# Kernel tuning notes

Measured on AMD Instinct MI355X. Metric: run time of the kernel, lower is better.

Reference implementation:

```python
import jax, jax.numpy as jnp
import numpy as np

B, S, D, H = 1, 2048, 1024, 16
DH = D // H  # 64
ROPE_THETA = 10000.0


def _rope_tables(seq_len, half_dim, theta):
    inv = 1.0 / (theta ** (np.arange(0, half_dim, dtype=np.float32) / half_dim))
    ang = np.arange(seq_len, dtype=np.float32)[:, None] * inv[None, :]
    return jnp.asarray(np.cos(ang)), jnp.asarray(np.sin(ang))


def setup_inputs() -> dict:
    key = jax.random.key(0)
    ks = jax.random.split(key, 6)
    x = jax.random.normal(ks[0], (B, S, D), dtype=jnp.float32)
    # block-diagonal mask over ~4 packed images -> sorted segment ids
    seg_ids = jnp.sort(jax.random.randint(ks[1], (S,), 0, 4, dtype=jnp.int32))
    freqs_cos, freqs_sin = _rope_tables(S, DH // 2, ROPE_THETA)
    scale = 1.0 / np.sqrt(D)
    wq = jax.random.normal(ks[2], (D, D), dtype=jnp.float32) * scale
    wk = jax.random.normal(ks[3], (D, D), dtype=jnp.float32) * scale
    wv = jax.random.normal(ks[4], (D, D), dtype=jnp.float32) * scale
    wo = jax.random.normal(ks[5], (D, D), dtype=jnp.float32) * scale
    return {"x": x, "seg_ids": seg_ids, "freqs_cos": freqs_cos,
            "freqs_sin": freqs_sin, "wq": wq, "wk": wk, "wv": wv, "wo": wo}


def _apply_rope(t, cos, sin):
    # t: [B,S,H,DH]; interpret last dim as DH//2 complex pairs (real, imag)
    tr = t.reshape(B, S, H, DH // 2, 2)
    a, b = tr[..., 0], tr[..., 1]
    c = cos[None, :, None, :]  # [1,S,1,DH/2]
    s = sin[None, :, None, :]
    out = jnp.stack([a * c - b * s, a * s + b * c], axis=-1)
    return out.reshape(B, S, H, DH)


def reference(x, seg_ids, freqs_cos, freqs_sin, wq, wk, wv, wo):
    q = (x @ wq.T).reshape(B, S, H, DH)
    k = (x @ wk.T).reshape(B, S, H, DH)
    v = (x @ wv.T).reshape(B, S, H, DH)
    q = _apply_rope(q, freqs_cos, freqs_sin)
    k = _apply_rope(k, freqs_cos, freqs_sin)
    scores = jnp.einsum('bqhd,bkhd->bhqk', q, k) / np.float32(np.sqrt(DH))
    block_mask = (seg_ids[:, None] == seg_ids[None, :])  # [S,S] block-diagonal
    scores = jnp.where(block_mask[None, None], scores, jnp.float32(-1e9))
    attn = jax.nn.softmax(scores, axis=-1)
    out = jnp.einsum('bhqk,bkhd->bqhd', attn, v).reshape(B, S, D)
    return out @ wo.T
```

## Files before the change

kernel.cpp:

```cpp
#include <hip/hip_runtime.h>

typedef __bf16 bf16;
typedef __bf16 bf16x4 __attribute__((ext_vector_type(4)));
typedef __bf16 bf16x8 __attribute__((ext_vector_type(8)));
typedef float  f32x4  __attribute__((ext_vector_type(4)));

#define S_LEN 2048
#define D_DIM 1024
#define NHEAD 16
#define DHEAD 64

__device__ __forceinline__ void async_cp16(const bf16* g, bf16* l) {
  __builtin_amdgcn_global_load_lds(
      (__attribute__((address_space(1))) void*)(void*)g,
      (__attribute__((address_space(3))) void*)l,
      16, 0, 0);
}

__global__ __launch_bounds__(256) void cvt_k(
    const float* __restrict__ x,  const float* __restrict__ w0,
    const float* __restrict__ w1, const float* __restrict__ w2,
    const float* __restrict__ w3, bf16* __restrict__ dst)
{
  int i = blockIdx.x * 256 + threadIdx.x;
  const float* src;
  int off;
  if (i < (1 << 18)) {
    src = x; off = i;
  } else {
    int j = i - (1 << 18);
    int s = j >> 17;
    off = j & ((1 << 17) - 1);
    src = (s == 0) ? w0 : (s == 1) ? w1 : (s == 2) ? w2 : w3;
  }
  f32x4 a = *(const f32x4*)(src + (size_t)off * 8);
  f32x4 b = *(const f32x4*)(src + (size_t)off * 8 + 4);
  bf16x8 o;
  o[0] = (bf16)a[0]; o[1] = (bf16)a[1]; o[2] = (bf16)a[2]; o[3] = (bf16)a[3];
  o[4] = (bf16)b[0]; o[5] = (bf16)b[1]; o[6] = (bf16)b[2]; o[7] = (bf16)b[3];
  *((bf16x8*)dst + i) = o;
}

template <typename OutT>
__global__ __launch_bounds__(256) void gemm_bt(
    const bf16* __restrict__ A,
    const bf16* __restrict__ B0, const bf16* __restrict__ B1,
    const bf16* __restrict__ B2,
    OutT* __restrict__ Cbase)
{
  constexpr int K = 1024, N = 1024;
  const int z = blockIdx.z;
  const bf16* W = (z == 0) ? B0 : (z == 1) ? B1 : B2;
  OutT* C = Cbase + (size_t)z * 2048 * 1024;

  __shared__ bf16 As[128 * 32] __attribute__((aligned(16)));
  __shared__ bf16 Bs[64 * 32] __attribute__((aligned(16)));

  const int t = threadIdx.x;
  const int lane = t & 63;
  const int w = t >> 6;
  const int lm = lane & 15, lq = lane >> 4;
  const int wr = w >> 1, wc = w & 1;
  const int bm = blockIdx.y, bn = blockIdx.x;

  const bf16* Abase = A + (size_t)bm * 128 * K;
  const bf16* Wbase = W + (size_t)bn * 64 * K;

  f32x4 acc[4][2] = {};

  for (int kk = 0; kk < K; kk += 32) {
#pragma unroll
    for (int i = 0; i < 2; ++i) {
      int c = w * 128 + i * 64 + lane;
      int row = c >> 2, kc = (c & 3) * 8;
      async_cp16(Abase + (size_t)row * K + kk + kc, As + (w * 2 + i) * 512);
    }
    {
      int c = w * 64 + lane;
      int row = c >> 2, kc = (c & 3) * 8;
      async_cp16(Wbase + (size_t)row * K + kk + kc, Bs + w * 512);
    }
    __syncthreads();

    bf16x8 af[4], bfr[2];
#pragma unroll
    for (int mi = 0; mi < 4; ++mi)
      af[mi] = *(const bf16x8*)&As[(wr * 64 + mi * 16 + lm) * 32 + lq * 8];
#pragma unroll
    for (int ni = 0; ni < 2; ++ni)
      bfr[ni] = *(const bf16x8*)&Bs[(wc * 32 + ni * 16 + lm) * 32 + lq * 8];
#pragma unroll
    for (int mi = 0; mi < 4; ++mi)
#pragma unroll
      for (int ni = 0; ni < 2; ++ni)
        acc[mi][ni] = __builtin_amdgcn_mfma_f32_16x16x32_bf16(
            af[mi], bfr[ni], acc[mi][ni], 0, 0, 0);
    __syncthreads();
  }

#pragma unroll
  for (int mi = 0; mi < 4; ++mi)
#pragma unroll
    for (int ni = 0; ni < 2; ++ni) {
      int col = bn * 64 + wc * 32 + ni * 16 + lm;
#pragma unroll
      for (int r = 0; r < 4; ++r) {
        int row = bm * 128 + wr * 64 + mi * 16 + lq * 4 + r;
        C[(size_t)row * N + col] = (OutT)acc[mi][ni][r];
      }
    }
}

__global__ __launch_bounds__(256) void prep_k(
    bf16* __restrict__ q, bf16* __restrict__ k,
    const bf16* __restrict__ v, bf16* __restrict__ vt,
    const float* __restrict__ cosT, const float* __restrict__ sinT,
    const int* __restrict__ seg, int* __restrict__ kbr)
{
  __shared__ bf16 tile[64 * 65];
  __shared__ int firstv[4];
  const int b = blockIdx.x;
  const int t = threadIdx.x;

  if (b < 1024) {
    bf16* ptr = (b < 512) ? q : k;
    float scale = (b < 512) ? 0.125f : 1.0f;
    int tid = (b & 511) * 256 + t;
    int s = tid >> 6;
    int u = tid & 63;
    int h = u >> 2, qq = u & 3;
    bf16* base = ptr + (size_t)s * D_DIM + h * DHEAD + qq * 16;
    bf16x8 lo = *(const bf16x8*)base;
    bf16x8 hi = *(const bf16x8*)(base + 8);
    f32x4 c0 = *(const f32x4*)(cosT + s * 32 + qq * 8);
    f32x4 c1 = *(const f32x4*)(cosT + s * 32 + qq * 8 + 4);
    f32x4 s0 = *(const f32x4*)(sinT + s * 32 + qq * 8);
    f32x4 s1 = *(const f32x4*)(sinT + s * 32 + qq * 8 + 4);
    bf16x8 olo, ohi;
#pragma unroll
    for (int j = 0; j < 4; ++j) {
      float a = (float)lo[2 * j], bb = (float)lo[2 * j + 1];
      olo[2 * j]     = (bf16)((a * c0[j] - bb * s0[j]) * scale);
      olo[2 * j + 1] = (bf16)((a * s0[j] + bb * c0[j]) * scale);
      float a2 = (float)hi[2 * j], b2 = (float)hi[2 * j + 1];
      ohi[2 * j]     = (bf16)((a2 * c1[j] - b2 * s1[j]) * scale);
      ohi[2 * j + 1] = (bf16)((a2 * s1[j] + b2 * c1[j]) * scale);
    }
    *(bf16x8*)base = olo;
    *(bf16x8*)(base + 8) = ohi;
  } else if (b < 1536) {
    int b2 = b - 1024;
    const int s0t = (b2 & 31) * 64;
    const int d0t = (b2 >> 5) * 64;
    const int c = t & 63, r0 = t >> 6;
#pragma unroll
    for (int r = r0; r < 64; r += 4)
      tile[r * 65 + c] = v[(size_t)(s0t + r) * D_DIM + d0t + c];
    __syncthreads();
#pragma unroll
    for (int r = r0; r < 64; r += 4)
      vt[(size_t)(d0t + r) * S_LEN + s0t + c] = tile[c * 65 + r];
  } else {
    if (t < 4) firstv[t] = S_LEN;
    __syncthreads();
    for (int i = t; i < S_LEN; i += 256) {
      int s = seg[i];
      if (i == 0 || seg[i - 1] != s) atomicMin(&firstv[s], i);
    }
    __syncthreads();
    if (t < 32) {
      int smin = seg[t * 64], smax = seg[t * 64 + 63];
      int lb = S_LEN, ub = S_LEN;
      for (int vv = smin; vv < 4; ++vv) lb = min(lb, firstv[vv]);
      for (int vv = smax + 1; vv < 4; ++vv) ub = min(ub, firstv[vv]);
      kbr[t * 2] = lb >> 6;
      kbr[t * 2 + 1] = (ub - 1) >> 6;
    }
  }
}

__global__ __launch_bounds__(256) void attn_k(
    const bf16* __restrict__ Q, const bf16* __restrict__ Kmat,
    const bf16* __restrict__ Vt, const int* __restrict__ seg,
    const int* __restrict__ kbr,
    float* __restrict__ Opar, float* __restrict__ Lpar)
{
  __shared__ bf16 Ks[64 * 72] __attribute__((aligned(16)));
  __shared__ bf16 Vs[64 * 72] __attribute__((aligned(16)));
  __shared__ bf16 Ps[4][16 * 72] __attribute__((aligned(16)));
  __shared__ int segk[64];

  const int h = blockIdx.y;
  const int qt = blockIdx.x & 31, par = blockIdx.x >> 5;
  const int q0 = qt * 64;
  const int t = threadIdx.x, lane = t & 63, w = t >> 6;
  const int lm = lane & 15, lq = lane >> 4;
  const int qrow = q0 + w * 16;

  const int kb0f = kbr[qt * 2], kb1f = kbr[qt * 2 + 1];

  bf16x8 qf[2];
#pragma unroll
  for (int ks = 0; ks < 2; ++ks)
    qf[ks] = *(const bf16x8*)(Q + (size_t)(qrow + lm) * D_DIM + h * DHEAD +
                              ks * 32 + lq * 8);

  int sq[4];
  float l_i[4];
#pragma unroll
  for (int r = 0; r < 4; ++r) {
    sq[r] = seg[qrow + lq * 4 + r];
    l_i[r] = 0.0f;
  }
  f32x4 o[4] = {};

  const int srow0 = t >> 3, sch = (t & 7) * 8;
  const int srow1 = (256 + t) >> 3;

  const int kbS = kb0f + par;
  f32x4 pk0, pk1, pv0, pv1;
  int psg;
  if (kbS <= kb1f) {
    const int k0 = kbS * 64;
    pk0 = *(const f32x4*)(Kmat + (size_t)(k0 + srow0) * D_DIM + h * DHEAD + sch);
    pk1 = *(const f32x4*)(Kmat + (size_t)(k0 + srow1) * D_DIM + h * DHEAD + sch);
    pv0 = *(const f32x4*)(Vt + (size_t)(h * DHEAD + srow0) * S_LEN + k0 + sch);
    pv1 = *(const f32x4*)(Vt + (size_t)(h * DHEAD + srow1) * S_LEN + k0 + sch);
    if (t < 64) psg = seg[k0 + t];
  }

  for (int kb = kbS; kb <= kb1f; kb += 2) {
    __syncthreads();
    *(f32x4*)&Ks[srow0 * 72 + sch] = pk0;
    *(f32x4*)&Ks[srow1 * 72 + sch] = pk1;
    *(f32x4*)&Vs[srow0 * 72 + sch] = pv0;
    *(f32x4*)&Vs[srow1 * 72 + sch] = pv1;
    if (t < 64) segk[t] = psg;
    __syncthreads();

    if (kb + 2 <= kb1f) {
      const int k0 = (kb + 2) * 64;
      pk0 = *(const f32x4*)(Kmat + (size_t)(k0 + srow0) * D_DIM + h * DHEAD + sch);
      pk1 = *(const f32x4*)(Kmat + (size_t)(k0 + srow1) * D_DIM + h * DHEAD + sch);
      pv0 = *(const f32x4*)(Vt + (size_t)(h * DHEAD + srow0) * S_LEN + k0 + sch);
      pv1 = *(const f32x4*)(Vt + (size_t)(h * DHEAD + srow1) * S_LEN + k0 + sch);
      if (t < 64) psg = seg[k0 + t];
    }

    f32x4 sa[4] = {};
#pragma unroll
    for (int ks = 0; ks < 2; ++ks) {
      bf16x8 kf[4];
#pragma unroll
      for (int ni = 0; ni < 4; ++ni)
        kf[ni] = *(const bf16x8*)&Ks[(ni * 16 + lm) * 72 + ks * 32 + lq * 8];
#pragma unroll
      for (int ni = 0; ni < 4; ++ni)
        sa[ni] = __builtin_amdgcn_mfma_f32_16x16x32_bf16(qf[ks], kf[ni],
                                                         sa[ni], 0, 0, 0);
    }

    int sk[4];
#pragma unroll
    for (int ni = 0; ni < 4; ++ni) sk[ni] = segk[ni * 16 + lm];

#pragma unroll
    for (int r = 0; r < 4; ++r)
#pragma unroll
      for (int ni = 0; ni < 4; ++ni) {
        float p = (sq[r] == sk[ni]) ? __expf(sa[ni][r]) : 0.0f;
        l_i[r] += p;
        Ps[w][(lq * 4 + r) * 72 + ni * 16 + lm] = (bf16)p;
      }

#pragma unroll
    for (int ks = 0; ks < 2; ++ks) {
      bf16x8 pf = *(const bf16x8*)&Ps[w][lm * 72 + ks * 32 + lq * 8];
      bf16x8 vf[4];
#pragma unroll
      for (int ni = 0; ni < 4; ++ni)
        vf[ni] = *(const bf16x8*)&Vs[(ni * 16 + lm) * 72 + ks * 32 + lq * 8];
#pragma unroll
      for (int ni = 0; ni < 4; ++ni)
        o[ni] = __builtin_amdgcn_mfma_f32_16x16x32_bf16(pf, vf[ni], o[ni],
                                                        0, 0, 0);
    }
  }

  float* Ob = Opar + ((size_t)(par * NHEAD + h) * S_LEN) * DHEAD;
  float* Lb = Lpar + (size_t)(par * NHEAD + h) * S_LEN;
#pragma unroll
  for (int r = 0; r < 4; ++r) {
    float l = l_i[r];
    l += __shfl_xor(l, 1);
    l += __shfl_xor(l, 2);
    l += __shfl_xor(l, 4);
    l += __shfl_xor(l, 8);
    int row = qrow + lq * 4 + r;
    if (lm == 0) Lb[row] = l;
#pragma unroll
    for (int ni = 0; ni < 4; ++ni)
      Ob[(size_t)row * DHEAD + ni * 16 + lm] = o[ni][r];
  }
}

__global__ __launch_bounds__(256) void combine_k(
    const float* __restrict__ Opar, const float* __restrict__ Lpar,
    bf16* __restrict__ AO)
{
  int idx = blockIdx.x * 256 + threadIdx.x;
  int c4 = idx & 15;
  int rh = idx >> 4;
  int row = rh & 2047;
  int h = rh >> 11;
  const size_t PO = (size_t)NHEAD * S_LEN * DHEAD;
  const float* o0 = Opar + ((size_t)h * S_LEN + row) * DHEAD + c4 * 4;
  f32x4 a = *(const f32x4*)o0;
  f32x4 b = *(const f32x4*)(o0 + PO);
  float l = Lpar[(size_t)h * S_LEN + row] +
            Lpar[(size_t)NHEAD * S_LEN + (size_t)h * S_LEN + row];
  float inv = 1.0f / l;
  bf16x4 ov;
#pragma unroll
  for (int j = 0; j < 4; ++j) ov[j] = (bf16)((a[j] + b[j]) * inv);
  *(bf16x4*)(AO + (size_t)row * D_DIM + h * DHEAD + c4 * 4) = ov;
}

extern "C" void kernel_launch(void* const* d_in, const int* in_sizes, int n_in,
                              void* d_out, int out_size, void* d_ws,
                              size_t ws_size, hipStream_t stream)
{
  const float* x  = (const float*)d_in[0];
  const int*   sg = (const int*)d_in[1];
  const float* fc = (const float*)d_in[2];
  const float* fs = (const float*)d_in[3];
  const float* wq = (const float*)d_in[4];
  const float* wk = (const float*)d_in[5];
  const float* wv = (const float*)d_in[6];
  const float* wo = (const float*)d_in[7];
  float* out = (float*)d_out;

  const size_t MAT = (size_t)S_LEN * D_DIM;
  const size_t WSZ = (size_t)D_DIM * D_DIM;
  bf16* xb  = (bf16*)d_ws;
  bf16* wqb = xb + MAT;
  bf16* wkb = wqb + WSZ;
  bf16* wvb = wkb + WSZ;
  bf16* wob = wvb + WSZ;
  bf16* q0  = wob + WSZ;
  bf16* k0  = q0 + MAT;
  bf16* v0  = k0 + MAT;
  bf16* vt  = v0 + MAT;
  bf16* ao  = vt + MAT;
  float* opar = (float*)(ao + MAT);
  float* lpar = opar + 2 * MAT;
  int*   kbr  = (int*)(lpar + 2 * NHEAD * S_LEN);

  dim3 blk(256);
  cvt_k<<<dim3(3072), blk, 0, stream>>>(x, wq, wk, wv, wo, xb);
  gemm_bt<bf16><<<dim3(16, 16, 3), blk, 0, stream>>>(xb, wqb, wkb, wvb, q0);
  prep_k<<<dim3(1537), blk, 0, stream>>>(q0, k0, v0, vt, fc, fs, sg, kbr);
  attn_k<<<dim3(64, 16), blk, 0, stream>>>(q0, k0, vt, sg, kbr, opar, lpar);
  combine_k<<<dim3(2048), blk, 0, stream>>>(opar, lpar, ao);
  gemm_bt<float><<<dim3(16, 16, 1), blk, 0, stream>>>(ao, wob, wob, wob, out);
}
```

Before: 158.5 us.

## Fuse RoPE into QKV GEMM epilogue, widen K-step, split-K output projection

RoPE rotation and the Q scale move into the QKV GEMM epilogue, using a lane shuffle to fetch the paired column, so the separate read-modify-write pass over Q and K is gone. Both GEMMs now stage 64-wide K chunks in two LDS buffers per barrier, which halves the number of sync points. The output projection is split-K over two z-slices and accumulates with fp32 atomics into a zeroed output, doubling its grid to fill more CUs. The cost is an extra memset plus atomic traffic and a nondeterministic summation order.

```diff
diff --git a/kernel.cpp b/kernel.cpp
--- a/kernel.cpp
+++ b/kernel.cpp
@@ -41,20 +41,22 @@
   *((bf16x8*)dst + i) = o;
 }
 
-template <typename OutT>
-__global__ __launch_bounds__(256) void gemm_bt(
+__global__ __launch_bounds__(256) void gemm_qkv(
     const bf16* __restrict__ A,
     const bf16* __restrict__ B0, const bf16* __restrict__ B1,
     const bf16* __restrict__ B2,
-    OutT* __restrict__ Cbase)
+    const float* __restrict__ cosT, const float* __restrict__ sinT,
+    bf16* __restrict__ Cbase)
 {
   constexpr int K = 1024, N = 1024;
   const int z = blockIdx.z;
   const bf16* W = (z == 0) ? B0 : (z == 1) ? B1 : B2;
-  OutT* C = Cbase + (size_t)z * 2048 * 1024;
-
-  __shared__ bf16 As[128 * 32] __attribute__((aligned(16)));
-  __shared__ bf16 Bs[64 * 32] __attribute__((aligned(16)));
+  bf16* C = Cbase + (size_t)z * 2048 * 1024;
+
+  __shared__ bf16 As0[128 * 32] __attribute__((aligned(16)));
+  __shared__ bf16 As1[128 * 32] __attribute__((aligned(16)));
+  __shared__ bf16 Bs0[64 * 32] __attribute__((aligned(16)));
+  __shared__ bf16 Bs1[64 * 32] __attribute__((aligned(16)));
 
   const int t = threadIdx.x;
   const int lane = t & 63;
@@ -68,33 +70,140 @@
 
   f32x4 acc[4][2] = {};
 
-  for (int kk = 0; kk < K; kk += 32) {
-#pragma unroll
-    for (int i = 0; i < 2; ++i) {
-      int c = w * 128 + i * 64 + lane;
-      int row = c >> 2, kc = (c & 3) * 8;
-      async_cp16(Abase + (size_t)row * K + kk + kc, As + (w * 2 + i) * 512);
+  for (int kk = 0; kk < K; kk += 64) {
+#pragma unroll
+    for (int g = 0; g < 2; ++g) {
+      int c = (w * 2 + g) * 64 + lane;
+      int row = c >> 2, k8 = c & 3;
+      const bf16* ga = Abase + (size_t)row * K + kk + k8 * 8;
+      async_cp16(ga, As0 + (w * 2 + g) * 512);
+      async_cp16(ga + 32, As1 + (w * 2 + g) * 512);
     }
     {
       int c = w * 64 + lane;
-      int row = c >> 2, kc = (c & 3) * 8;
-      async_cp16(Wbase + (size_t)row * K + kk + kc, Bs + w * 512);
-    }
-    __syncthreads();
-
-    bf16x8 af[4], bfr[2];
+      int row = c >> 2, k8 = c & 3;
+      const bf16* gb = Wbase + (size_t)row * K + kk + k8 * 8;
+      async_cp16(gb, Bs0 + w * 512);
+      async_cp16(gb + 32, Bs1 + w * 512);
+    }
+    __syncthreads();
+
+#pragma unroll
+    for (int ks = 0; ks < 2; ++ks) {
+      const bf16* As = ks ? As1 : As0;
+      const bf16* Bs = ks ? Bs1 : Bs0;
+      bf16x8 af[4], bfr[2];
+#pragma unroll
+      for (int mi = 0; mi < 4; ++mi)
+        af[mi] = *(const bf16x8*)&As[(wr * 64 + mi * 16 + lm) * 32 + lq * 8];
+#pragma unroll
+      for (int ni = 0; ni < 2; ++ni)
+        bfr[ni] = *(const bf16x8*)&Bs[(wc * 32 + ni * 16 + lm) * 32 + lq * 8];
+#pragma unroll
+      for (int mi = 0; mi < 4; ++mi)
+#pragma unroll
+        for (int ni = 0; ni < 2; ++ni)
+          acc[mi][ni] = __builtin_amdgcn_mfma_f32_16x16x32_bf16(
+              af[mi], bfr[ni], acc[mi][ni], 0, 0, 0);
+    }
+    __syncthreads();
+  }
+
+  if (z < 2) {
+    const float scale = (z == 0) ? 0.125f : 1.0f;
 #pragma unroll
     for (int mi = 0; mi < 4; ++mi)
-      af[mi] = *(const bf16x8*)&As[(wr * 64 + mi * 16 + lm) * 32 + lq * 8];
-#pragma unroll
-    for (int ni = 0; ni < 2; ++ni)
-      bfr[ni] = *(const bf16x8*)&Bs[(wc * 32 + ni * 16 + lm) * 32 + lq * 8];
+#pragma unroll
+      for (int ni = 0; ni < 2; ++ni) {
+        int gcol = bn * 64 + wc * 32 + ni * 16 + lm;
+        int p = (gcol & 63) >> 1;
+        bool even = (gcol & 1) == 0;
+#pragma unroll
+        for (int r = 0; r < 4; ++r) {
+          int row = bm * 128 + wr * 64 + mi * 16 + lq * 4 + r;
+          float v = acc[mi][ni][r];
+          float mate = __shfl_xor(v, 1);
+          float cv = cosT[row * 32 + p];
+          float sv = sinT[row * 32 + p];
+          float res = even ? (v * cv - mate * sv) : (mate * sv + v * cv);
+          C[(size_t)row * N + gcol] = (bf16)(res * scale);
+        }
+      }
+  } else {
 #pragma unroll
     for (int mi = 0; mi < 4; ++mi)
 #pragma unroll
+      for (int ni = 0; ni < 2; ++ni) {
+        int gcol = bn * 64 + wc * 32 + ni * 16 + lm;
+#pragma unroll
+        for (int r = 0; r < 4; ++r) {
+          int row = bm * 128 + wr * 64 + mi * 16 + lq * 4 + r;
+          C[(size_t)row * N + gcol] = (bf16)acc[mi][ni][r];
+        }
+      }
+  }
+}
+
+__global__ __launch_bounds__(256) void gemm_wo(
+    const bf16* __restrict__ A, const bf16* __restrict__ W,
+    float* __restrict__ C)
+{
+  constexpr int K = 1024, N = 1024;
+  const int z = blockIdx.z;
+
+  __shared__ bf16 As0[128 * 32] __attribute__((aligned(16)));
+  __shared__ bf16 As1[128 * 32] __attribute__((aligned(16)));
+  __shared__ bf16 Bs0[64 * 32] __attribute__((aligned(16)));
+  __shared__ bf16 Bs1[64 * 32] __attribute__((aligned(16)));
+
+  const int t = threadIdx.x;
+  const int lane = t & 63;
+  const int w = t >> 6;
+  const int lm = lane & 15, lq = lane >> 4;
+  const int wr = w >> 1, wc = w & 1;
+  const int bm = blockIdx.y, bn = blockIdx.x;
+
+  const bf16* Abase = A + (size_t)bm * 128 * K;
+  const bf16* Wbase = W + (size_t)bn * 64 * K;
+
+  f32x4 acc[4][2] = {};
+
+  for (int kk = z * 512; kk < z * 512 + 512; kk += 64) {
+#pragma unroll
+    for (int g = 0; g < 2; ++g) {
+      int c = (w * 2 + g) * 64 + lane;
+      int row = c >> 2, k8 = c & 3;
+      const bf16* ga = Abase + (size_t)row * K + kk + k8 * 8;
+      async_cp16(ga, As0 + (w * 2 + g) * 512);
+      async_cp16(ga + 32, As1 + (w * 2 + g) * 512);
+    }
+    {
+      int c = w * 64 + lane;
+      int row = c >> 2, k8 = c & 3;
+      const bf16* gb = Wbase + (size_t)row * K + kk + k8 * 8;
+      async_cp16(gb, Bs0 + w * 512);
+      async_cp16(gb + 32, Bs1 + w * 512);
+    }
+    __syncthreads();
+
+#pragma unroll
+    for (int ks = 0; ks < 2; ++ks) {
+      const bf16* As = ks ? As1 : As0;
+      const bf16* Bs = ks ? Bs1 : Bs0;
+      bf16x8 af[4], bfr[2];
+#pragma unroll
+      for (int mi = 0; mi < 4; ++mi)
+        af[mi] = *(const bf16x8*)&As[(wr * 64 + mi * 16 + lm) * 32 + lq * 8];
+#pragma unroll
       for (int ni = 0; ni < 2; ++ni)
-        acc[mi][ni] = __builtin_amdgcn_mfma_f32_16x16x32_bf16(
-            af[mi], bfr[ni], acc[mi][ni], 0, 0, 0);
+        bfr[ni] = *(const bf16x8*)&Bs[(wc * 32 + ni * 16 + lm) * 32 + lq * 8];
+#pragma unroll
+      for (int mi = 0; mi < 4; ++mi)
+#pragma unroll
+        for (int ni = 0; ni < 2; ++ni)
+          acc[mi][ni] = __builtin_amdgcn_mfma_f32_16x16x32_bf16(
+              af[mi], bfr[ni], acc[mi][ni], 0, 0, 0);
+    }
     __syncthreads();
   }
 
@@ -106,15 +215,13 @@
 #pragma unroll
       for (int r = 0; r < 4; ++r) {
         int row = bm * 128 + wr * 64 + mi * 16 + lq * 4 + r;
-        C[(size_t)row * N + col] = (OutT)acc[mi][ni][r];
+        atomicAdd(&C[(size_t)row * N + col], acc[mi][ni][r]);
       }
     }
 }
 
 __global__ __launch_bounds__(256) void prep_k(
-    bf16* __restrict__ q, bf16* __restrict__ k,
     const bf16* __restrict__ v, bf16* __restrict__ vt,
-    const float* __restrict__ cosT, const float* __restrict__ sinT,
     const int* __restrict__ seg, int* __restrict__ kbr)
 {
   __shared__ bf16 tile[64 * 65];
@@ -122,36 +229,9 @@
   const int b = blockIdx.x;
   const int t = threadIdx.x;
 
-  if (b < 1024) {
-    bf16* ptr = (b < 512) ? q : k;
-    float scale = (b < 512) ? 0.125f : 1.0f;
-    int tid = (b & 511) * 256 + t;
-    int s = tid >> 6;
-    int u = tid & 63;
-    int h = u >> 2, qq = u & 3;
-    bf16* base = ptr + (size_t)s * D_DIM + h * DHEAD + qq * 16;
-    bf16x8 lo = *(const bf16x8*)base;
-    bf16x8 hi = *(const bf16x8*)(base + 8);
-    f32x4 c0 = *(const f32x4*)(cosT + s * 32 + qq * 8);
-    f32x4 c1 = *(const f32x4*)(cosT + s * 32 + qq * 8 + 4);
-    f32x4 s0 = *(const f32x4*)(sinT + s * 32 + qq * 8);
-    f32x4 s1 = *(const f32x4*)(sinT + s * 32 + qq * 8 + 4);
-    bf16x8 olo, ohi;
-#pragma unroll
-    for (int j = 0; j < 4; ++j) {
-      float a = (float)lo[2 * j], bb = (float)lo[2 * j + 1];
-      olo[2 * j]     = (bf16)((a * c0[j] - bb * s0[j]) * scale);
-      olo[2 * j + 1] = (bf16)((a * s0[j] + bb * c0[j]) * scale);
-      float a2 = (float)hi[2 * j], b2 = (float)hi[2 * j + 1];
-      ohi[2 * j]     = (bf16)((a2 * c1[j] - b2 * s1[j]) * scale);
-      ohi[2 * j + 1] = (bf16)((a2 * s1[j] + b2 * c1[j]) * scale);
-    }
-    *(bf16x8*)base = olo;
-    *(bf16x8*)(base + 8) = ohi;
-  } else if (b < 1536) {
-    int b2 = b - 1024;
-    const int s0t = (b2 & 31) * 64;
-    const int d0t = (b2 >> 5) * 64;
+  if (b < 512) {
+    const int s0t = (b & 31) * 64;
+    const int d0t = (b >> 5) * 64;
     const int c = t & 63, r0 = t >> 6;
 #pragma unroll
     for (int r = r0; r < 64; r += 4)
@@ -357,10 +437,11 @@
   int*   kbr  = (int*)(lpar + 2 * NHEAD * S_LEN);
 
   dim3 blk(256);
+  hipMemsetAsync(out, 0, (size_t)out_size * sizeof(float), stream);
   cvt_k<<<dim3(3072), blk, 0, stream>>>(x, wq, wk, wv, wo, xb);
-  gemm_bt<bf16><<<dim3(16, 16, 3), blk, 0, stream>>>(xb, wqb, wkb, wvb, q0);
-  prep_k<<<dim3(1537), blk, 0, stream>>>(q0, k0, v0, vt, fc, fs, sg, kbr);
+  gemm_qkv<<<dim3(16, 16, 3), blk, 0, stream>>>(xb, wqb, wkb, wvb, fc, fs, q0);
+  prep_k<<<dim3(513), blk, 0, stream>>>(v0, vt, sg, kbr);
   attn_k<<<dim3(64, 16), blk, 0, stream>>>(q0, k0, vt, sg, kbr, opar, lpar);
   combine_k<<<dim3(2048), blk, 0, stream>>>(opar, lpar, ao);
-  gemm_bt<float><<<dim3(16, 16, 1), blk, 0, stream>>>(ao, wob, wob, wob, out);
-}
+  gemm_wo<<<dim3(16, 16, 2), blk, 0, stream>>>(ao, wob, out);
+}
```

Result: no change. 160.2 us (+1.1%).
